# Performance work log

Measured on AMD Instinct MI355X. Metric: run time of the kernel, lower is better.

Reference implementation:

```python
import jax, jax.numpy as jnp
import numpy as np
from jax import lax

TOP_K = 2


def setup_inputs() -> dict:
    key = jax.random.key(0)
    ks = jax.random.split(key, 12)
    B, T, D, E, H = 8, 2048, 1024, 8, 4096
    LS = 1824  # router input size: D + 32 + D//4 + D//4 + D//8 + D//8
    s = 0.02
    return {
        "x": jax.random.normal(ks[0], (B, T, D), jnp.float32),
        "city_idx": 2,
        "delta_t_info": jax.random.normal(ks[1], (B, T, D // 4), jnp.float32),
        "delta_dis_info": jax.random.normal(ks[2], (B, T, D // 4), jnp.float32),
        "delta_rg_info": jax.random.normal(ks[3], (B, T, D // 8), jnp.float32),
        "delta_entropy_info": jax.random.normal(ks[4], (B, T, D // 8), jnp.float32),
        "city_embeddings": jax.random.normal(ks[5], (4, 32), jnp.float32),
        "W_route": jax.random.normal(ks[6], (LS, E), jnp.float32) * s,
        "b_route": jnp.zeros((E,), jnp.float32),
        "Wfc": jax.random.normal(ks[7], (E, D, H), jnp.float32) * s,
        "bfc": jnp.zeros((E, H), jnp.float32),
        "Wproj": jax.random.normal(ks[8], (E, H, D), jnp.float32) * s,
        "bproj": jnp.zeros((E, D), jnp.float32),
    }


def reference(x, city_idx, delta_t_info, delta_dis_info, delta_rg_info,
              delta_entropy_info, city_embeddings, W_route, b_route,
              Wfc, bfc, Wproj, bproj):
    B, T, D = x.shape
    E = W_route.shape[-1]
    # --- NoisyTopkRouter (eval path: no noise) ---
    ce = jnp.broadcast_to(city_embeddings[city_idx], (B, T, 32))
    feat = jnp.concatenate(
        [x, ce, delta_t_info, delta_dis_info, delta_rg_info, delta_entropy_info], axis=-1)
    logits = feat @ W_route + b_route            # [B,T,E]
    gate1 = jax.nn.softmax(logits, axis=-1)
    top_vals, top_idx = lax.top_k(logits, TOP_K)  # [B,T,k]
    N = B * T
    flat_sparse = jnp.full((N, E), -jnp.inf, dtype=logits.dtype)
    rows = jnp.arange(N)[:, None]
    flat_sparse = flat_sparse.at[rows, top_idx.reshape(N, TOP_K)].set(
        top_vals.reshape(N, TOP_K))
    gating = jax.nn.softmax(flat_sparse, axis=-1).reshape(B, T, E)  # zero off top-k
    # --- Experts: gating is exactly zero for non-selected experts, so the
    # masked gather/scatter in torch equals a gate-weighted dense sum. ---
    out = jnp.zeros_like(x)
    for e in range(E):
        h = jax.nn.gelu(x @ Wfc[e] + bfc[e], approximate=True)  # tanh GELU
        out = out + (h @ Wproj[e] + bproj[e]) * gating[..., e:e + 1]
    return out, gate1
```

## Files before the change

### kernel.cpp

```cpp
#include <hip/hip_runtime.h>
#include <hip/hip_bf16.h>
#include <math.h>

#define B_       8
#define T_       2048
#define N_TOK    (B_*T_)
#define D_       1024
#define E_       8
#define H_       4096
#define TOPK     2
#define R_       (N_TOK*TOPK)
#define OUT_ELEMS ((size_t)N_TOK*D_)

#define BM 128
#define BN 128
#define BK 32
#define MAXT 264
#define NPH 3
#define TPP 88
#define HROWS (TPP*BM)

typedef __attribute__((ext_vector_type(8))) short short8;
typedef __attribute__((ext_vector_type(4))) float floatx4;
typedef const __attribute__((address_space(1))) void* gptr_t;
typedef __attribute__((address_space(3))) void* lptr_t;

__device__ __forceinline__ void gl16(const void* g, void* l) {
  __builtin_amdgcn_global_load_lds((gptr_t)g, (lptr_t)l, 16, 0, 0);
}

__device__ __forceinline__ unsigned short f2bf(float f) {
  union { float f; unsigned int u; } v; v.f = f;
  unsigned int u = v.u;
  u += 0x7FFFu + ((u >> 16) & 1u);
  return (unsigned short)(u >> 16);
}

__device__ __forceinline__ float gelu_tanh(float v) {
  float c = v + 0.044715f * v * v * v;
  return 0.5f * v * (1.0f + tanhf(0.7978845608028654f * c));
}

__global__ __launch_bounds__(256) void router_kernel(
    const float* __restrict__ x, const int* __restrict__ city_idx_p,
    const float* __restrict__ dt, const float* __restrict__ dd,
    const float* __restrict__ drg, const float* __restrict__ de,
    const float* __restrict__ cemb, const float* __restrict__ Wr,
    const float* __restrict__ br,
    float* __restrict__ gate1, int* __restrict__ topk_e,
    float* __restrict__ topk_w)
{
  const int wid = threadIdx.x >> 6, lane = threadIdx.x & 63;
  const int token = blockIdx.x * 4 + wid;

  float acc[E_];
#pragma unroll
  for (int e = 0; e < E_; e++) acc[e] = 0.f;

  const float* ce = cemb + (*city_idx_p) * 32;

  auto fma_seg4 = [&](const float* src, int ng, int base) {
    for (int i = lane; i < ng; i += 64) {
      float4 f = ((const float4*)src)[i];
      const float4* wv = (const float4*)(Wr + (size_t)(base + i * 4) * E_);
      float4 w0 = wv[0], w1 = wv[1], w2 = wv[2], w3 = wv[3];
      float4 w4 = wv[4], w5 = wv[5], w6 = wv[6], w7 = wv[7];
      acc[0] += f.x * w0.x; acc[1] += f.x * w0.y; acc[2] += f.x * w0.z; acc[3] += f.x * w0.w;
      acc[4] += f.x * w1.x; acc[5] += f.x * w1.y; acc[6] += f.x * w1.z; acc[7] += f.x * w1.w;
      acc[0] += f.y * w2.x; acc[1] += f.y * w2.y; acc[2] += f.y * w2.z; acc[3] += f.y * w2.w;
      acc[4] += f.y * w3.x; acc[5] += f.y * w3.y; acc[6] += f.y * w3.z; acc[7] += f.y * w3.w;
      acc[0] += f.z * w4.x; acc[1] += f.z * w4.y; acc[2] += f.z * w4.z; acc[3] += f.z * w4.w;
      acc[4] += f.z * w5.x; acc[5] += f.z * w5.y; acc[6] += f.z * w5.z; acc[7] += f.z * w5.w;
      acc[0] += f.w * w6.x; acc[1] += f.w * w6.y; acc[2] += f.w * w6.z; acc[3] += f.w * w6.w;
      acc[4] += f.w * w7.x; acc[5] += f.w * w7.y; acc[6] += f.w * w7.z; acc[7] += f.w * w7.w;
    }
  };
  fma_seg4(x  + (size_t)token * D_,  D_ / 4, 0);
  fma_seg4(ce,                       32 / 4, 1024);
  fma_seg4(dt + (size_t)token * 256, 256 / 4, 1056);
  fma_seg4(dd + (size_t)token * 256, 256 / 4, 1312);
  fma_seg4(drg+ (size_t)token * 128, 128 / 4, 1568);
  fma_seg4(de + (size_t)token * 128, 128 / 4, 1696);

#pragma unroll
  for (int e = 0; e < E_; e++) {
    float v = acc[e];
#pragma unroll
    for (int s = 32; s > 0; s >>= 1) v += __shfl_xor(v, s, 64);
    acc[e] = v + br[e];
  }

  if (lane == 0) {
    float mx = acc[0];
#pragma unroll
    for (int e = 1; e < E_; e++) mx = fmaxf(mx, acc[e]);
    float s = 0.f, ex[E_];
#pragma unroll
    for (int e = 0; e < E_; e++) { ex[e] = expf(acc[e] - mx); s += ex[e]; }
    float inv = 1.f / s;
#pragma unroll
    for (int e = 0; e < E_; e++) gate1[(size_t)token * E_ + e] = ex[e] * inv;

    int e0 = 0;
#pragma unroll
    for (int e = 1; e < E_; e++) if (acc[e] > acc[e0]) e0 = e;
    int e1 = (e0 == 0) ? 1 : 0;
#pragma unroll
    for (int e = 0; e < E_; e++) if (e != e0 && acc[e] > acc[e1]) e1 = e;
    float t2 = expf(acc[e1] - acc[e0]);
    float w0 = 1.f / (1.f + t2), w1 = t2 / (1.f + t2);
    topk_e[token * 2]     = e0; topk_e[token * 2 + 1] = e1;
    topk_w[token * 2]     = w0; topk_w[token * 2 + 1] = w1;
  }
}

__global__ __launch_bounds__(256) void hist_kernel(const int* __restrict__ topk_e,
                                                   int* __restrict__ counts)
{
  __shared__ int h[E_];
  const int t = threadIdx.x;
  if (t < E_) h[t] = 0;
  __syncthreads();
  const int base = blockIdx.x * 1024 + t;
#pragma unroll
  for (int j = 0; j < 4; j++) atomicAdd(&h[topk_e[base + j * 256]], 1);
  __syncthreads();
  if (t < E_ && h[t] > 0) atomicAdd(&counts[t], h[t]);
}

__global__ void build_tiles_kernel(const int* __restrict__ counts, int* pbase,
                                   int* cursors, int* tile_expert, int* num_tiles)
{
  if (threadIdx.x == 0 && blockIdx.x == 0) {
    int t = 0;
    for (int e = 0; e < E_; e++) {
      pbase[e] = t * BM;
      cursors[e] = 0;
      int nt = (counts[e] + BM - 1) / BM;
      for (int i = 0; i < nt; i++) tile_expert[t++] = e;
    }
    *num_tiles = t;
  }
}

__global__ __launch_bounds__(256) void scatter_kernel(
    const int* __restrict__ topk_e, const float* __restrict__ topk_w,
    const int* __restrict__ pbase, int* __restrict__ cursors,
    int* __restrict__ prow_token, float* __restrict__ prow_w)
{
  __shared__ int wcnt[4][E_];
  __shared__ int wbase[4][E_];
  const int t = threadIdx.x, lane = t & 63, wid = t >> 6;
  if (t < 32) ((int*)wcnt)[t] = 0;
  __syncthreads();

  const int idx = blockIdx.x * 256 + t;
  const int e = topk_e[idx];
  const float w = topk_w[idx];

  unsigned long long b0 = __ballot(e & 1);
  unsigned long long b1 = __ballot(e & 2);
  unsigned long long b2 = __ballot(e & 4);
  unsigned long long m = ((e & 1) ? b0 : ~b0) & ((e & 2) ? b1 : ~b1) & ((e & 4) ? b2 : ~b2);
  unsigned long long below = ((unsigned long long)1 << lane) - 1;
  const int rank = __popcll(m & below);
  if (rank == 0) wcnt[wid][e] = __popcll(m);
  __syncthreads();

  if (t < E_) {
    int run = 0, tmp[4];
#pragma unroll
    for (int w2 = 0; w2 < 4; w2++) { tmp[w2] = run; run += wcnt[w2][t]; }
    int gb = (run > 0) ? atomicAdd(&cursors[t], run) : 0;
#pragma unroll
    for (int w2 = 0; w2 < 4; w2++) wbase[w2][t] = gb + tmp[w2];
  }
  __syncthreads();

  const int pos = pbase[e] + wbase[wid][e] + rank;
  prow_token[pos] = idx >> 1;
  prow_w[pos] = w;
}

__global__ __launch_bounds__(256) void xconv_kernel(const float* __restrict__ x,
                                                    unsigned short* __restrict__ xbf)
{
  size_t i = ((size_t)blockIdx.x * 256 + threadIdx.x) * 8;
  float4 a = ((const float4*)(x + i))[0], b = ((const float4*)(x + i))[1];
  unsigned short o[8] = {f2bf(a.x), f2bf(a.y), f2bf(a.z), f2bf(a.w),
                         f2bf(b.x), f2bf(b.y), f2bf(b.z), f2bf(b.w)};
  *(short8*)(xbf + i) = *(short8*)o;
}

__global__ __launch_bounds__(256) void wtrans_kernel(
    const float* __restrict__ W, unsigned short* __restrict__ Wt, int K, int N)
{
  const int e = blockIdx.z, k0 = blockIdx.x * 32, n0 = blockIdx.y * 128;
  __shared__ unsigned short Ls[128 * 40];
  const int t = threadIdx.x;
  const int kr = t >> 3;
  const int cg = (t & 7) * 16;
  const float* src = W + ((size_t)e * K + k0 + kr) * N + n0 + cg;
  float4 f0 = ((const float4*)src)[0];
  float4 f1 = ((const float4*)src)[1];
  float4 f2 = ((const float4*)src)[2];
  float4 f3 = ((const float4*)src)[3];
  float v[16] = {f0.x,f0.y,f0.z,f0.w, f1.x,f1.y,f1.z,f1.w,
                 f2.x,f2.y,f2.z,f2.w, f3.x,f3.y,f3.z,f3.w};
#pragma unroll
  for (int j = 0; j < 16; j++) Ls[(cg + j) * 40 + kr] = f2bf(v[j]);
  __syncthreads();
  const int r = t >> 1, hh = (t & 1) * 16;
  unsigned short* dst = Wt + ((size_t)e * N + n0 + r) * K + k0 + hh;
  short8 o0 = *(short8*)&Ls[r * 40 + hh];
  short8 o1 = *(short8*)&Ls[r * 40 + hh + 8];
  *(short8*)dst       = o0;
  *(short8*)(dst + 8) = o1;
}

__global__ __launch_bounds__(256) void fc_gemm_kernel(
    const unsigned short* __restrict__ xbf, const unsigned short* __restrict__ Wt,
    const float* __restrict__ bfc, const int* __restrict__ prow_token,
    const int* __restrict__ tile_expert, const int* __restrict__ num_tiles_p,
    const unsigned short* __restrict__ zrow,
    unsigned short* __restrict__ H, int tile_base)
{
  const int tile = tile_base + blockIdx.y;
  if (tile >= *num_tiles_p) return;
  const int e  = tile_expert[tile];
  const int n0 = blockIdx.x * BN;
  const int ltile = tile - tile_base;

  __shared__ unsigned short As[BM * BK];
  __shared__ unsigned short Bs[BN * BK];
  __shared__ int toks[BM];

  const int t = threadIdx.x;
  if (t < BM) toks[t] = prow_token[tile * BM + t];
  __syncthreads();

  const int lane = t & 63, wid = t >> 6;
  const int ko = (lane & 3) * 8;
  const int r0 = wid * 32 + (lane >> 2);
  const int tk0 = toks[r0], tk1 = toks[r0 + 16];
  const unsigned short* pa0 = (tk0 >= 0) ? xbf + (size_t)tk0 * D_ + ko : zrow + ko;
  const unsigned short* pa1 = (tk1 >= 0) ? xbf + (size_t)tk1 * D_ + ko : zrow + ko;
  const unsigned short* WtE = Wt + (size_t)e * H_ * D_;
  const unsigned short* pb0 = WtE + (size_t)(n0 + r0) * D_ + ko;
  const unsigned short* pb1 = pb0 + (size_t)16 * D_;
  unsigned short* lA0 = &As[wid * 1024];
  unsigned short* lA1 = &As[wid * 1024 + 512];
  unsigned short* lB0 = &Bs[wid * 1024];
  unsigned short* lB1 = &Bs[wid * 1024 + 512];

  const int wm = (wid >> 1) * 64, wn = (wid & 1) * 64;
  const int lrow = lane & 15, quad = lane >> 4;

  floatx4 acc[4][4];
#pragma unroll
  for (int i = 0; i < 4; i++)
#pragma unroll
    for (int j = 0; j < 4; j++) acc[i][j] = (floatx4){0.f, 0.f, 0.f, 0.f};

  for (int k0 = 0; k0 < D_; k0 += BK) {
    gl16(pa0 + k0, lA0);
    gl16(pa1 + k0, lA1);
    gl16(pb0 + k0, lB0);
    gl16(pb1 + k0, lB1);
    __syncthreads();

    short8 af[4], bfr[4];
#pragma unroll
    for (int mi = 0; mi < 4; mi++)
      af[mi]  = *(const short8*)&As[(wm + mi * 16 + lrow) * BK + quad * 8];
#pragma unroll
    for (int ni = 0; ni < 4; ni++)
      bfr[ni] = *(const short8*)&Bs[(wn + ni * 16 + lrow) * BK + quad * 8];
#pragma unroll
    for (int mi = 0; mi < 4; mi++)
#pragma unroll
      for (int ni = 0; ni < 4; ni++)
        acc[mi][ni] = __builtin_amdgcn_mfma_f32_16x16x32_bf16(af[mi], bfr[ni], acc[mi][ni], 0, 0, 0);
    __syncthreads();
  }

  const float* bias = bfc + (size_t)e * H_ + n0;
#pragma unroll
  for (int mi = 0; mi < 4; mi++) {
    int row = wm + mi * 16 + quad * 4;
#pragma unroll
    for (int ni = 0; ni < 4; ni++) {
      int col = wn + ni * 16 + lrow;
      float b = bias[col];
#pragma unroll
      for (int r = 0; r < 4; r++) {
        float v = acc[mi][ni][r] + b;
        H[(size_t)(ltile * BM + row + r) * H_ + n0 + col] = f2bf(gelu_tanh(v));
      }
    }
  }
}

__global__ __launch_bounds__(256) void proj_gemm_kernel(
    const unsigned short* __restrict__ H, const unsigned short* __restrict__ Wt,
    const float* __restrict__ bpj, const int* __restrict__ prow_token,
    const float* __restrict__ prow_w, const int* __restrict__ tile_expert,
    const int* __restrict__ num_tiles_p, float* __restrict__ out, int tile_base)
{
  const int tile = tile_base + blockIdx.y;
  if (tile >= *num_tiles_p) return;
  const int e  = tile_expert[tile];
  const int n0 = blockIdx.x * BN;
  const int ltile = tile - tile_base;

  __shared__ unsigned short As[BM * BK];
  __shared__ unsigned short Bs[BN * BK];
  __shared__ int   toks[BM];
  __shared__ float wgt[BM];

  const int t = threadIdx.x;
  if (t < BM) { toks[t] = prow_token[tile * BM + t]; wgt[t] = prow_w[tile * BM + t]; }
  __syncthreads();

  const int lane = t & 63, wid = t >> 6;
  const int ko = (lane & 3) * 8;
  const int r0 = wid * 32 + (lane >> 2);
  const unsigned short* pa0 = H + (size_t)(ltile * BM + r0) * H_ + ko;
  const unsigned short* pa1 = pa0 + (size_t)16 * H_;
  const unsigned short* WtE = Wt + (size_t)e * D_ * H_;
  const unsigned short* pb0 = WtE + (size_t)(n0 + r0) * H_ + ko;
  const unsigned short* pb1 = pb0 + (size_t)16 * H_;
  unsigned short* lA0 = &As[wid * 1024];
  unsigned short* lA1 = &As[wid * 1024 + 512];
  unsigned short* lB0 = &Bs[wid * 1024];
  unsigned short* lB1 = &Bs[wid * 1024 + 512];

  const int wm = (wid >> 1) * 64, wn = (wid & 1) * 64;
  const int lrow = lane & 15, quad = lane >> 4;

  floatx4 acc[4][4];
#pragma unroll
  for (int i = 0; i < 4; i++)
#pragma unroll
    for (int j = 0; j < 4; j++) acc[i][j] = (floatx4){0.f, 0.f, 0.f, 0.f};

  for (int k0 = 0; k0 < H_; k0 += BK) {
    gl16(pa0 + k0, lA0);
    gl16(pa1 + k0, lA1);
    gl16(pb0 + k0, lB0);
    gl16(pb1 + k0, lB1);
    __syncthreads();

    short8 af[4], bfr[4];
#pragma unroll
    for (int mi = 0; mi < 4; mi++)
      af[mi]  = *(const short8*)&As[(wm + mi * 16 + lrow) * BK + quad * 8];
#pragma unroll
    for (int ni = 0; ni < 4; ni++)
      bfr[ni] = *(const short8*)&Bs[(wn + ni * 16 + lrow) * BK + quad * 8];
#pragma unroll
    for (int mi = 0; mi < 4; mi++)
#pragma unroll
      for (int ni = 0; ni < 4; ni++)
        acc[mi][ni] = __builtin_amdgcn_mfma_f32_16x16x32_bf16(af[mi], bfr[ni], acc[mi][ni], 0, 0, 0);
    __syncthreads();
  }

  const float* bias = bpj + (size_t)e * D_ + n0;
#pragma unroll
  for (int mi = 0; mi < 4; mi++) {
    int row = wm + mi * 16 + quad * 4;
#pragma unroll
    for (int ni = 0; ni < 4; ni++) {
      int col = wn + ni * 16 + lrow;
      float b = bias[col];
#pragma unroll
      for (int r = 0; r < 4; r++) {
        int rr = row + r;
        int tok = toks[rr];
        if (tok >= 0) {
          float v = (acc[mi][ni][r] + b) * wgt[rr];
          atomicAdd(&out[(size_t)tok * D_ + n0 + col], v);
        }
      }
    }
  }
}

extern "C" void kernel_launch(void* const* d_in, const int* in_sizes, int n_in,
                              void* d_out, int out_size, void* d_ws, size_t ws_size,
                              hipStream_t stream)
{
  const float* x    = (const float*)d_in[0];
  const int*   cidx = (const int*)d_in[1];
  const float* dt   = (const float*)d_in[2];
  const float* dd   = (const float*)d_in[3];
  const float* drg  = (const float*)d_in[4];
  const float* de   = (const float*)d_in[5];
  const float* cemb = (const float*)d_in[6];
  const float* Wr   = (const float*)d_in[7];
  const float* br   = (const float*)d_in[8];
  const float* Wfc  = (const float*)d_in[9];
  const float* bfc  = (const float*)d_in[10];
  const float* Wpj  = (const float*)d_in[11];
  const float* bpj  = (const float*)d_in[12];

  float* out   = (float*)d_out;
  float* gate1 = out + OUT_ELEMS;

  char* ws = (char*)d_ws;
  size_t off = 0;
  auto take = [&](size_t bytes) { size_t r = off; off += (bytes + 255) & ~(size_t)255; return r; };
  unsigned short* Hbuf  = (unsigned short*)(ws + take((size_t)HROWS * H_ * 2));
  unsigned short* xbf   = (unsigned short*)(ws + take((size_t)N_TOK * D_ * 2));
  unsigned short* WtFc  = (unsigned short*)(ws + take((size_t)E_ * H_ * D_ * 2));
  unsigned short* WtPj  = (unsigned short*)(ws + take((size_t)E_ * D_ * H_ * 2));
  int*   topk_e      = (int*)  (ws + take((size_t)R_ * 4));
  float* topk_w      = (float*)(ws + take((size_t)R_ * 4));
  int*   prow_token  = (int*)  (ws + take((size_t)(MAXT * BM) * 4));
  float* prow_w      = (float*)(ws + take((size_t)(MAXT * BM) * 4));
  unsigned short* zrow = (unsigned short*)(ws + take(4096));
  int*   counts      = (int*)  (ws + take(E_ * 4));
  int*   cursors     = (int*)  (ws + take(E_ * 4));
  int*   pbase       = (int*)  (ws + take(E_ * 4));
  int*   tile_expert = (int*)  (ws + take(MAXT * 4));
  int*   num_tiles   = (int*)  (ws + take(4));
  (void)ws_size; (void)in_sizes; (void)n_in; (void)out_size;

  hipMemsetAsync(d_out, 0, OUT_ELEMS * 4, stream);
  hipMemsetAsync(counts, 0, E_ * 4, stream);
  hipMemsetAsync(prow_token, 0xFF, (size_t)(MAXT * BM) * 4, stream);
  hipMemsetAsync(zrow, 0, 4096, stream);

  xconv_kernel<<<(N_TOK * D_) / (256 * 8), 256, 0, stream>>>(x, xbf);
  wtrans_kernel<<<dim3(D_ / 32, H_ / 128, E_), 256, 0, stream>>>(Wfc, WtFc, D_, H_);
  wtrans_kernel<<<dim3(H_ / 32, D_ / 128, E_), 256, 0, stream>>>(Wpj, WtPj, H_, D_);

  router_kernel<<<N_TOK / 4, 256, 0, stream>>>(x, cidx, dt, dd, drg, de, cemb, Wr, br,
                                               gate1, topk_e, topk_w);
  hist_kernel<<<R_ / 1024, 256, 0, stream>>>(topk_e, counts);
  build_tiles_kernel<<<1, 64, 0, stream>>>(counts, pbase, cursors, tile_expert, num_tiles);
  scatter_kernel<<<R_ / 256, 256, 0, stream>>>(topk_e, topk_w, pbase, cursors, prow_token, prow_w);

  for (int p = 0; p < NPH; p++) {
    int base = p * TPP;
    fc_gemm_kernel<<<dim3(H_ / BN, TPP), 256, 0, stream>>>(xbf, WtFc, bfc, prow_token,
                                                           tile_expert, num_tiles, zrow,
                                                           Hbuf, base);
    proj_gemm_kernel<<<dim3(D_ / BN, TPP), 256, 0, stream>>>(Hbuf, WtPj, bpj, prow_token,
                                                             prow_w, tile_expert, num_tiles,
                                                             out, base);
  }
}
```

Baseline: 1.506 ms.

## Double K-step per barrier in expert GEMMs and use fast exp2-based GELU

Both expert GEMM kernels now load two 32-wide K panels into shared memory per iteration and run MFMAs on both before syncing. This halves the number of barriers and load-wait phases per tile, at the cost of twice the LDS footprint. The tanh GELU is rewritten as x*sigmoid(2c) using the hardware exp2 and reciprocal intrinsics, replacing tanhf in the FC epilogue. This is mathematically equivalent up to approximation error.

```diff
diff --git a/kernel.cpp b/kernel.cpp
--- a/kernel.cpp
+++ b/kernel.cpp
@@ -15,6 +15,8 @@
 #define BM 128
 #define BN 128
 #define BK 32
+#define KSTEP 64
+#define PANEL (BM*BK)
 #define MAXT 264
 #define NPH 3
 #define TPP 88
@@ -37,8 +39,9 @@
 }
 
 __device__ __forceinline__ float gelu_tanh(float v) {
-  float c = v + 0.044715f * v * v * v;
-  return 0.5f * v * (1.0f + tanhf(0.7978845608028654f * c));
+  float u = __builtin_fmaf(v * v, -0.10294325f, -2.30220830f);
+  float p = __builtin_amdgcn_exp2f(v * u);
+  return v * __builtin_amdgcn_rcpf(1.0f + p);
 }
 
 __global__ __launch_bounds__(256) void router_kernel(
@@ -231,8 +234,8 @@
   const int n0 = blockIdx.x * BN;
   const int ltile = tile - tile_base;
 
-  __shared__ unsigned short As[BM * BK];
-  __shared__ unsigned short Bs[BN * BK];
+  __shared__ unsigned short As[2 * PANEL];
+  __shared__ unsigned short Bs[2 * PANEL];
   __shared__ int toks[BM];
 
   const int t = threadIdx.x;
@@ -262,25 +265,32 @@
 #pragma unroll
     for (int j = 0; j < 4; j++) acc[i][j] = (floatx4){0.f, 0.f, 0.f, 0.f};
 
-  for (int k0 = 0; k0 < D_; k0 += BK) {
-    gl16(pa0 + k0, lA0);
-    gl16(pa1 + k0, lA1);
-    gl16(pb0 + k0, lB0);
-    gl16(pb1 + k0, lB1);
+  for (int k0 = 0; k0 < D_; k0 += KSTEP) {
+    gl16(pa0 + k0,      lA0);
+    gl16(pa1 + k0,      lA1);
+    gl16(pb0 + k0,      lB0);
+    gl16(pb1 + k0,      lB1);
+    gl16(pa0 + k0 + 32, lA0 + PANEL);
+    gl16(pa1 + k0 + 32, lA1 + PANEL);
+    gl16(pb0 + k0 + 32, lB0 + PANEL);
+    gl16(pb1 + k0 + 32, lB1 + PANEL);
     __syncthreads();
 
-    short8 af[4], bfr[4];
-#pragma unroll
-    for (int mi = 0; mi < 4; mi++)
-      af[mi]  = *(const short8*)&As[(wm + mi * 16 + lrow) * BK + quad * 8];
-#pragma unroll
-    for (int ni = 0; ni < 4; ni++)
-      bfr[ni] = *(const short8*)&Bs[(wn + ni * 16 + lrow) * BK + quad * 8];
-#pragma unroll
-    for (int mi = 0; mi < 4; mi++)
+#pragma unroll
+    for (int kk = 0; kk < 2; kk++) {
+      short8 af[4], bfr[4];
+#pragma unroll
+      for (int mi = 0; mi < 4; mi++)
+        af[mi]  = *(const short8*)&As[kk * PANEL + (wm + mi * 16 + lrow) * BK + quad * 8];
 #pragma unroll
       for (int ni = 0; ni < 4; ni++)
-        acc[mi][ni] = __builtin_amdgcn_mfma_f32_16x16x32_bf16(af[mi], bfr[ni], acc[mi][ni], 0, 0, 0);
+        bfr[ni] = *(const short8*)&Bs[kk * PANEL + (wn + ni * 16 + lrow) * BK + quad * 8];
+#pragma unroll
+      for (int mi = 0; mi < 4; mi++)
+#pragma unroll
+        for (int ni = 0; ni < 4; ni++)
+          acc[mi][ni] = __builtin_amdgcn_mfma_f32_16x16x32_bf16(af[mi], bfr[ni], acc[mi][ni], 0, 0, 0);
+    }
     __syncthreads();
   }
 
@@ -313,8 +323,8 @@
   const int n0 = blockIdx.x * BN;
   const int ltile = tile - tile_base;
 
-  __shared__ unsigned short As[BM * BK];
-  __shared__ unsigned short Bs[BN * BK];
+  __shared__ unsigned short As[2 * PANEL];
+  __shared__ unsigned short Bs[2 * PANEL];
   __shared__ int   toks[BM];
   __shared__ float wgt[BM];
 
@@ -344,25 +354,32 @@
 #pragma unroll
     for (int j = 0; j < 4; j++) acc[i][j] = (floatx4){0.f, 0.f, 0.f, 0.f};
 
-  for (int k0 = 0; k0 < H_; k0 += BK) {
-    gl16(pa0 + k0, lA0);
-    gl16(pa1 + k0, lA1);
-    gl16(pb0 + k0, lB0);
-    gl16(pb1 + k0, lB1);
+  for (int k0 = 0; k0 < H_; k0 += KSTEP) {
+    gl16(pa0 + k0,      lA0);
+    gl16(pa1 + k0,      lA1);
+    gl16(pb0 + k0,      lB0);
+    gl16(pb1 + k0,      lB1);
+    gl16(pa0 + k0 + 32, lA0 + PANEL);
+    gl16(pa1 + k0 + 32, lA1 + PANEL);
+    gl16(pb0 + k0 + 32, lB0 + PANEL);
+    gl16(pb1 + k0 + 32, lB1 + PANEL);
     __syncthreads();
 
-    short8 af[4], bfr[4];
-#pragma unroll
-    for (int mi = 0; mi < 4; mi++)
-      af[mi]  = *(const short8*)&As[(wm + mi * 16 + lrow) * BK + quad * 8];
-#pragma unroll
-    for (int ni = 0; ni < 4; ni++)
-      bfr[ni] = *(const short8*)&Bs[(wn + ni * 16 + lrow) * BK + quad * 8];
-#pragma unroll
-    for (int mi = 0; mi < 4; mi++)
+#pragma unroll
+    for (int kk = 0; kk < 2; kk++) {
+      short8 af[4], bfr[4];
+#pragma unroll
+      for (int mi = 0; mi < 4; mi++)
+        af[mi]  = *(const short8*)&As[kk * PANEL + (wm + mi * 16 + lrow) * BK + quad * 8];
 #pragma unroll
       for (int ni = 0; ni < 4; ni++)
-        acc[mi][ni] = __builtin_amdgcn_mfma_f32_16x16x32_bf16(af[mi], bfr[ni], acc[mi][ni], 0, 0, 0);
+        bfr[ni] = *(const short8*)&Bs[kk * PANEL + (wn + ni * 16 + lrow) * BK + quad * 8];
+#pragma unroll
+      for (int mi = 0; mi < 4; mi++)
+#pragma unroll
+        for (int ni = 0; ni < 4; ni++)
+          acc[mi][ni] = __builtin_amdgcn_mfma_f32_16x16x32_bf16(af[mi], bfr[ni], acc[mi][ni], 0, 0, 0);
+    }
     __syncthreads();
   }
 
```

New measurement: 1.688 ms. +12.1%, slower.

## Split-K proj GEMM, remap block IDs across XCDs, and use fast exp-based GELU

Applied to the files above, without the earlier changes.

The proj GEMM grid gains a z dimension that splits the K=4096 reduction into two halves. The existing atomicAdd epilogue accumulates both partials, and the bias is added only once. Both GEMMs remap the linear block index with a stride-8 permutation so consecutive blocks land on the same XCD, which should improve L2 reuse of shared weight tiles. GELU tanh is rewritten as x*sigmoid(2c) using hardware exp2 and rcp intrinsics, trading a little precision for fewer instructions in the epilogue.

```diff
diff --git a/kernel.cpp b/kernel.cpp
--- a/kernel.cpp
+++ b/kernel.cpp
@@ -37,8 +37,9 @@
 }
 
 __device__ __forceinline__ float gelu_tanh(float v) {
-  float c = v + 0.044715f * v * v * v;
-  return 0.5f * v * (1.0f + tanhf(0.7978845608028654f * c));
+  float u = __builtin_fmaf(v * v, -0.10294325f, -2.30220830f);
+  float p = __builtin_amdgcn_exp2f(v * u);
+  return v * __builtin_amdgcn_rcpf(1.0f + p);
 }
 
 __global__ __launch_bounds__(256) void router_kernel(
@@ -225,10 +226,15 @@
     const unsigned short* __restrict__ zrow,
     unsigned short* __restrict__ H, int tile_base)
 {
-  const int tile = tile_base + blockIdx.y;
+  const int s  = blockIdx.y * 32 + blockIdx.x;
+  const int w  = (s & 7) * ((32 * TPP) >> 3) + (s >> 3);
+  const int bx = w & 31;
+  const int by = w >> 5;
+
+  const int tile = tile_base + by;
   if (tile >= *num_tiles_p) return;
   const int e  = tile_expert[tile];
-  const int n0 = blockIdx.x * BN;
+  const int n0 = bx * BN;
   const int ltile = tile - tile_base;
 
   __shared__ unsigned short As[BM * BK];
@@ -307,10 +313,17 @@
     const float* __restrict__ prow_w, const int* __restrict__ tile_expert,
     const int* __restrict__ num_tiles_p, float* __restrict__ out, int tile_base)
 {
-  const int tile = tile_base + blockIdx.y;
+  const int s  = blockIdx.x + (blockIdx.y << 3) + blockIdx.z * (8 * TPP);
+  const int w  = (s & 7) * ((8 * TPP * 2) >> 3) + (s >> 3);
+  const int z  = (w >= 8 * TPP) ? 1 : 0;
+  const int rem = w - z * (8 * TPP);
+  const int bx = rem & 7;
+  const int by = rem >> 3;
+
+  const int tile = tile_base + by;
   if (tile >= *num_tiles_p) return;
   const int e  = tile_expert[tile];
-  const int n0 = blockIdx.x * BN;
+  const int n0 = bx * BN;
   const int ltile = tile - tile_base;
 
   __shared__ unsigned short As[BM * BK];
@@ -344,7 +357,8 @@
 #pragma unroll
     for (int j = 0; j < 4; j++) acc[i][j] = (floatx4){0.f, 0.f, 0.f, 0.f};
 
-  for (int k0 = 0; k0 < H_; k0 += BK) {
+  const int kbeg = z * (H_ / 2), kend = kbeg + (H_ / 2);
+  for (int k0 = kbeg; k0 < kend; k0 += BK) {
     gl16(pa0 + k0, lA0);
     gl16(pa1 + k0, lA1);
     gl16(pb0 + k0, lB0);
@@ -373,7 +387,7 @@
 #pragma unroll
     for (int ni = 0; ni < 4; ni++) {
       int col = wn + ni * 16 + lrow;
-      float b = bias[col];
+      float b = z ? 0.f : bias[col];
 #pragma unroll
       for (int r = 0; r < 4; r++) {
         int rr = row + r;
@@ -447,8 +461,8 @@
     fc_gemm_kernel<<<dim3(H_ / BN, TPP), 256, 0, stream>>>(xbf, WtFc, bfc, prow_token,
                                                            tile_expert, num_tiles, zrow,
                                                            Hbuf, base);
-    proj_gemm_kernel<<<dim3(D_ / BN, TPP), 256, 0, stream>>>(Hbuf, WtPj, bpj, prow_token,
-                                                             prow_w, tile_expert, num_tiles,
-                                                             out, base);
-  }
-}
+    proj_gemm_kernel<<<dim3(D_ / BN, TPP, 2), 256, 0, stream>>>(Hbuf, WtPj, bpj, prow_token,
+                                                                prow_w, tile_expert, num_tiles,
+                                                                out, base);
+  }
+}
```

Result: no change. 1.531 ms (+1.7%).
